# Kernel optimization log

Hardware: AMD Instinct MI355X
Metric: run time of the kernel (lower is better)

Reference implementation:

```python
import jax, jax.numpy as jnp
import numpy as np

N, E, D = 100000, 640000, 128  # nodes, edges, feature dim (in_dim == out_dim == 128)
BN_EPS = 1e-5


def setup_inputs() -> dict:
    key = jax.random.key(0)
    ks = jax.random.split(key, 8)
    x = jax.random.normal(ks[0], (N, D), dtype=jnp.float32)
    edge_index = jax.random.randint(ks[1], (2, E), 0, N, dtype=jnp.int64)
    s = 1.0 / np.sqrt(D)
    W1 = jax.random.uniform(ks[2], (D, D), jnp.float32, -s, s)
    b1 = jax.random.uniform(ks[3], (D,), jnp.float32, -s, s)
    W2 = jax.random.uniform(ks[4], (D, D), jnp.float32, -s, s)
    b2 = jax.random.uniform(ks[5], (D,), jnp.float32, -s, s)
    return {
        "x": x,
        "edge_index": edge_index,
        "eps": jnp.array([0.1], dtype=jnp.float32),
        "W1": W1, "b1": b1,
        "g1": jnp.ones((D,), jnp.float32), "beta1": jnp.zeros((D,), jnp.float32),
        "W2": W2, "b2": b2,
        "g2": jnp.ones((D,), jnp.float32), "beta2": jnp.zeros((D,), jnp.float32),
    }


def _batchnorm(h, gamma, beta):
    # BatchNorm1d in training mode: biased batch stats over the node dim
    mean = jnp.mean(h, axis=0)
    var = jnp.var(h, axis=0)
    return gamma * (h - mean) * jax.lax.rsqrt(var + BN_EPS) + beta


def reference(x, edge_index, eps, W1, b1, g1, beta1, W2, b2, g2, beta2):
    src, dst = edge_index[0], edge_index[1]
    # gather messages from source nodes, scatter-add into destination nodes
    aggr = jax.ops.segment_sum(x[src], dst, num_segments=x.shape[0])  # [N, D]
    h = (1.0 + eps) * x + aggr
    h = jax.nn.relu(_batchnorm(h @ W1.T + b1, g1, beta1))
    h = jax.nn.relu(_batchnorm(h @ W2.T + b2, g2, beta2))
    return h
```

## Files before the change

kernel.cpp:

```cpp
#include <hip/hip_runtime.h>

#define NN 100000
#define DD 128
#define EE 640000
#define NPAD 100352

typedef __bf16 bf16x8 __attribute__((ext_vector_type(8)));
typedef float floatx4 __attribute__((ext_vector_type(4)));

__device__ __forceinline__ unsigned short f2bf(float f) {
    unsigned int u = __float_as_uint(f);
    u += 0x7FFF + ((u >> 16) & 1);
    return (unsigned short)(u >> 16);
}

__global__ __launch_bounds__(256) void hist_k(const int* __restrict__ ei,
                                              int* __restrict__ deg) {
    int e = blockIdx.x * 256 + threadIdx.x;
    if (e < EE) atomicAdd(&deg[ei[EE + e]], 1);
}

__global__ __launch_bounds__(256) void scan1_k(const int* __restrict__ deg,
                                               int* __restrict__ exc,
                                               int* __restrict__ chunkSums) {
    __shared__ int s[256];
    int t = threadIdx.x, g = blockIdx.x * 256 + t;
    int v = (g < NN) ? deg[g] : 0;
    s[t] = v;
    __syncthreads();
    for (int off = 1; off < 256; off <<= 1) {
        int u = (t >= off) ? s[t - off] : 0;
        __syncthreads();
        s[t] += u;
        __syncthreads();
    }
    if (g < NN) exc[g] = s[t] - v;
    if (t == 255) chunkSums[blockIdx.x] = s[255];
}

__global__ __launch_bounds__(512) void scan2_k(int* __restrict__ chunkSums, int n) {
    __shared__ int s[512];
    int t = threadIdx.x;
    int v = (t < n) ? chunkSums[t] : 0;
    s[t] = v;
    __syncthreads();
    for (int off = 1; off < 512; off <<= 1) {
        int u = (t >= off) ? s[t - off] : 0;
        __syncthreads();
        s[t] += u;
        __syncthreads();
    }
    if (t < n) chunkSums[t] = s[t] - v;
}

__global__ __launch_bounds__(256) void scan3_k(int* __restrict__ exc,
                                               const int* __restrict__ chunkSums,
                                               int* __restrict__ cursor) {
    int g = blockIdx.x * 256 + threadIdx.x;
    if (g < NN) {
        int o = exc[g] + chunkSums[blockIdx.x];
        exc[g] = o;
        cursor[g] = o;
    }
}

__global__ __launch_bounds__(256) void esort_k(const int* __restrict__ ei,
                                               int* __restrict__ cursor,
                                               int* __restrict__ ssrc) {
    int e = blockIdx.x * 256 + threadIdx.x;
    if (e >= EE) return;
    int pos = atomicAdd(&cursor[ei[EE + e]], 1);
    ssrc[pos] = ei[e];
}

__global__ __launch_bounds__(256) void aggregate_k(
    const float4* __restrict__ x4, const int* __restrict__ ssrc,
    const int* __restrict__ offs, const int* __restrict__ deg,
    const float* __restrict__ epsp, ushort4* __restrict__ hout) {
    int tid = blockIdx.x * 256 + threadIdx.x;
    int node = tid >> 5, lane = tid & 31;
    if (node >= NN) return;
    int start = offs[node], d = deg[node];
    float ef = 1.0f + epsp[0];
    float4 v = x4[node * 32 + lane];
    float4 acc = make_float4(ef * v.x, ef * v.y, ef * v.z, ef * v.w);
    for (int j = 0; j < d; ++j) {
        int s = ssrc[start + j];
        float4 xv = x4[s * 32 + lane];
        acc.x += xv.x; acc.y += xv.y; acc.z += xv.z; acc.w += xv.w;
    }
    ushort4 u;
    u.x = f2bf(acc.x); u.y = f2bf(acc.y); u.z = f2bf(acc.z); u.w = f2bf(acc.w);
    hout[node * 32 + lane] = u;
}

__global__ __launch_bounds__(256, 2) void gin_gemm_k(
    const unsigned short* __restrict__ hin,
    const float* __restrict__ W, const float* __restrict__ bias,
    float* __restrict__ y, float* __restrict__ stats) {
    __shared__ __align__(16) unsigned short Ah[128][136];
    __shared__ __align__(16) unsigned short Bw[128][136];
    __shared__ __align__(16) float s_sum[128];
    __shared__ __align__(16) float s_sq[128];

    const int tid = threadIdx.x;
    const int rowBase = blockIdx.x * 128;

    if (tid < 128) { s_sum[tid] = 0.f; s_sq[tid] = 0.f; }

    const float4* W4 = (const float4*)W;
#pragma unroll
    for (int j = 0; j < 16; ++j) {
        int f4 = j * 256 + tid;
        int row = f4 >> 5, k4 = f4 & 31;
        float4 wv = W4[f4];
        ushort4 u;
        u.x = f2bf(wv.x); u.y = f2bf(wv.y); u.z = f2bf(wv.z); u.w = f2bf(wv.w);
        *(ushort4*)&Bw[row][k4 * 4] = u;
    }

    const int4* h16 = (const int4*)hin;
#pragma unroll
    for (int j = 0; j < 8; ++j) {
        int c = j * 256 + tid;
        int row = c >> 4, c8 = c & 15;
        int rg = rowBase + row;
        int4 v = make_int4(0, 0, 0, 0);
        if (rg < NN) v = h16[rg * 16 + c8];
        *(int4*)&Ah[row][c8 * 8] = v;
    }

    __syncthreads();

    const int l = tid & 63, w = tid >> 6;
    const int m = l & 15, q = l >> 4;

    floatx4 acc[2][8];
#pragma unroll
    for (int rt = 0; rt < 2; ++rt)
#pragma unroll
        for (int ct = 0; ct < 8; ++ct) acc[rt][ct] = (floatx4)0.0f;

#pragma unroll
    for (int kc = 0; kc < 4; ++kc) {
        int k0 = kc * 32 + q * 8;
        bf16x8 a0 = *(const bf16x8*)&Ah[w * 32 + m][k0];
        bf16x8 a1 = *(const bf16x8*)&Ah[w * 32 + 16 + m][k0];
#pragma unroll
        for (int ct = 0; ct < 8; ++ct) {
            bf16x8 b = *(const bf16x8*)&Bw[ct * 16 + m][k0];
            acc[0][ct] = __builtin_amdgcn_mfma_f32_16x16x32_bf16(a0, b, acc[0][ct], 0, 0, 0);
            acc[1][ct] = __builtin_amdgcn_mfma_f32_16x16x32_bf16(a1, b, acc[1][ct], 0, 0, 0);
        }
    }

#pragma unroll
    for (int ct = 0; ct < 8; ++ct) {
        int col = ct * 16 + m;
        float bc = bias[col];
        float ps = 0.f, pq = 0.f;
#pragma unroll
        for (int rt = 0; rt < 2; ++rt) {
#pragma unroll
            for (int i = 0; i < 4; ++i) {
                int rg = rowBase + w * 32 + rt * 16 + q * 4 + i;
                if (rg < NN) {
                    float yv = acc[rt][ct][i] + bc;
                    y[rg * 128 + col] = yv;
                    ps += yv;
                    pq += yv * yv;
                }
            }
        }
        atomicAdd(&s_sum[col], ps);
        atomicAdd(&s_sq[col], pq);
    }
    __syncthreads();
    if (tid < 128) {
        unsafeAtomicAdd(&stats[tid], s_sum[tid]);
        unsafeAtomicAdd(&stats[128 + tid], s_sq[tid]);
    }
}

template <int OUT_BF16>
__global__ __launch_bounds__(256) void bn_relu_k(
    const float* __restrict__ y, const float* __restrict__ stats,
    const float* __restrict__ g, const float* __restrict__ beta,
    float* outf, unsigned short* __restrict__ outh) {
    __shared__ __align__(16) float sc[128];
    __shared__ __align__(16) float sh[128];
    int t = threadIdx.x;
    if (t < 128) {
        const float inv = 1.0f / (float)NN;
        float mean = stats[t] * inv;
        float var = stats[128 + t] * inv - mean * mean;
        float s = g[t] * rsqrtf(var + 1e-5f);
        sc[t] = s;
        sh[t] = beta[t] - mean * s;
    }
    __syncthreads();
    const int total4 = NN * 32;
    const float4* y4 = (const float4*)y;
    for (int i = blockIdx.x * 256 + t; i < total4; i += gridDim.x * 256) {
        int c4 = i & 31;
        float4 v = y4[i];
        float4 s = ((const float4*)sc)[c4];
        float4 b = ((const float4*)sh)[c4];
        float r0 = fmaxf(v.x * s.x + b.x, 0.f);
        float r1 = fmaxf(v.y * s.y + b.y, 0.f);
        float r2 = fmaxf(v.z * s.z + b.z, 0.f);
        float r3 = fmaxf(v.w * s.w + b.w, 0.f);
        if (OUT_BF16) {
            ushort4 u;
            u.x = f2bf(r0); u.y = f2bf(r1); u.z = f2bf(r2); u.w = f2bf(r3);
            ((ushort4*)outh)[i] = u;
        } else {
            ((float4*)outf)[i] = make_float4(r0, r1, r2, r3);
        }
    }
}

extern "C" void kernel_launch(void* const* d_in, const int* in_sizes, int n_in,
                              void* d_out, int out_size, void* d_ws, size_t ws_size,
                              hipStream_t stream) {
    const float* x   = (const float*)d_in[0];
    const int* ei    = (const int*)d_in[1];
    const float* W1  = (const float*)d_in[3];
    const float* b1  = (const float*)d_in[4];
    const float* g1  = (const float*)d_in[5];
    const float* be1 = (const float*)d_in[6];
    const float* W2  = (const float*)d_in[7];
    const float* b2  = (const float*)d_in[8];
    const float* g2  = (const float*)d_in[9];
    const float* be2 = (const float*)d_in[10];
    const float* eps = (const float*)d_in[2];
    float* out = (float*)d_out;

    int* deg        = (int*)d_ws;
    int* offs       = deg + NPAD;
    int* cursor     = offs + NPAD;
    int* chunkSums  = cursor + NPAD;
    int* ssrc       = chunkSums + 512;
    unsigned short* hbuf = (unsigned short*)(ssrc + EE + 256);
    float* stats    = (float*)(hbuf + (size_t)NN * DD);

    hipMemsetAsync(deg, 0, NPAD * sizeof(int), stream);
    hipMemsetAsync(stats, 0, 512 * sizeof(float), stream);

    const int numChunks = (NN + 255) / 256;
    hist_k<<<(EE + 255) / 256, 256, 0, stream>>>(ei, deg);
    scan1_k<<<numChunks, 256, 0, stream>>>(deg, offs, chunkSums);
    scan2_k<<<1, 512, 0, stream>>>(chunkSums, numChunks);
    scan3_k<<<numChunks, 256, 0, stream>>>(offs, chunkSums, cursor);
    esort_k<<<(EE + 255) / 256, 256, 0, stream>>>(ei, cursor, ssrc);
    aggregate_k<<<(NN * 32 + 255) / 256, 256, 0, stream>>>(
        (const float4*)x, ssrc, offs, deg, eps, (ushort4*)hbuf);

    int gblocks = (NN + 127) / 128;
    gin_gemm_k<<<gblocks, 256, 0, stream>>>(hbuf, W1, b1, out, stats);
    bn_relu_k<1><<<4096, 256, 0, stream>>>(out, stats, g1, be1, nullptr, hbuf);
    gin_gemm_k<<<gblocks, 256, 0, stream>>>(hbuf, W2, b2, out, stats + 256);
    bn_relu_k<0><<<4096, 256, 0, stream>>>(out, stats + 256, g2, be2, out, nullptr);
}
```

Baseline: 361.2 us.

## Fuse first BN+ReLU into second GEMM load and unroll gather by four

```diff
diff --git a/kernel.cpp b/kernel.cpp
--- a/kernel.cpp
+++ b/kernel.cpp
@@ -83,30 +83,62 @@
     int start = offs[node], d = deg[node];
     float ef = 1.0f + epsp[0];
     float4 v = x4[node * 32 + lane];
-    float4 acc = make_float4(ef * v.x, ef * v.y, ef * v.z, ef * v.w);
-    for (int j = 0; j < d; ++j) {
-        int s = ssrc[start + j];
-        float4 xv = x4[s * 32 + lane];
-        acc.x += xv.x; acc.y += xv.y; acc.z += xv.z; acc.w += xv.w;
+    float ax = ef * v.x, ay = ef * v.y, az = ef * v.z, aw = ef * v.w;
+    for (int j = 0; j < d; j += 4) {
+        int r = d - j;
+        int b = start + j;
+        int s0 = ssrc[b];
+        int s1 = ssrc[b + ((r > 1) ? 1 : 0)];
+        int s2 = ssrc[b + ((r > 2) ? 2 : 0)];
+        int s3 = ssrc[b + ((r > 3) ? 3 : 0)];
+        float4 xa = x4[s0 * 32 + lane];
+        float4 xb = x4[s1 * 32 + lane];
+        float4 xc = x4[s2 * 32 + lane];
+        float4 xd = x4[s3 * 32 + lane];
+        float m1 = (r > 1) ? 1.f : 0.f;
+        float m2 = (r > 2) ? 1.f : 0.f;
+        float m3 = (r > 3) ? 1.f : 0.f;
+        ax += xa.x; ay += xa.y; az += xa.z; aw += xa.w;
+        ax += m1 * xb.x; ay += m1 * xb.y; az += m1 * xb.z; aw += m1 * xb.w;
+        ax += m2 * xc.x; ay += m2 * xc.y; az += m2 * xc.z; aw += m2 * xc.w;
+        ax += m3 * xd.x; ay += m3 * xd.y; az += m3 * xd.z; aw += m3 * xd.w;
     }
     ushort4 u;
-    u.x = f2bf(acc.x); u.y = f2bf(acc.y); u.z = f2bf(acc.z); u.w = f2bf(acc.w);
+    u.x = f2bf(ax); u.y = f2bf(ay); u.z = f2bf(az); u.w = f2bf(aw);
     hout[node * 32 + lane] = u;
 }
 
+template <int FUSE_BN>
 __global__ __launch_bounds__(256, 2) void gin_gemm_k(
     const unsigned short* __restrict__ hin,
+    const float* __restrict__ yin,
+    const float* __restrict__ statsIn,
+    const float* __restrict__ gmm,
+    const float* __restrict__ bta,
     const float* __restrict__ W, const float* __restrict__ bias,
-    float* __restrict__ y, float* __restrict__ stats) {
+    float* __restrict__ y, float* __restrict__ statsOut) {
     __shared__ __align__(16) unsigned short Ah[128][136];
     __shared__ __align__(16) unsigned short Bw[128][136];
     __shared__ __align__(16) float s_sum[128];
     __shared__ __align__(16) float s_sq[128];
+    __shared__ __align__(16) float sc[128];
+    __shared__ __align__(16) float sh[128];
 
     const int tid = threadIdx.x;
     const int rowBase = blockIdx.x * 128;
 
-    if (tid < 128) { s_sum[tid] = 0.f; s_sq[tid] = 0.f; }
+    if (tid < 128) {
+        s_sum[tid] = 0.f;
+        s_sq[tid] = 0.f;
+        if (FUSE_BN) {
+            const float inv = 1.0f / (float)NN;
+            float mean = statsIn[tid] * inv;
+            float var = statsIn[128 + tid] * inv - mean * mean;
+            float s = gmm[tid] * rsqrtf(var + 1e-5f);
+            sc[tid] = s;
+            sh[tid] = bta[tid] - mean * s;
+        }
+    }
 
     const float4* W4 = (const float4*)W;
 #pragma unroll
@@ -119,15 +151,37 @@
         *(ushort4*)&Bw[row][k4 * 4] = u;
     }
 
-    const int4* h16 = (const int4*)hin;
-#pragma unroll
-    for (int j = 0; j < 8; ++j) {
-        int c = j * 256 + tid;
-        int row = c >> 4, c8 = c & 15;
-        int rg = rowBase + row;
-        int4 v = make_int4(0, 0, 0, 0);
-        if (rg < NN) v = h16[rg * 16 + c8];
-        *(int4*)&Ah[row][c8 * 8] = v;
+    if (FUSE_BN) {
+        __syncthreads();
+        const float4* y4in = (const float4*)yin;
+#pragma unroll
+        for (int j = 0; j < 16; ++j) {
+            int c = j * 256 + tid;
+            int row = c >> 5, c4 = c & 31;
+            int rg = rowBase + row;
+            ushort4 u = make_ushort4(0, 0, 0, 0);
+            if (rg < NN) {
+                float4 v = y4in[rg * 32 + c4];
+                float4 s4 = ((const float4*)sc)[c4];
+                float4 b4 = ((const float4*)sh)[c4];
+                u.x = f2bf(fmaxf(v.x * s4.x + b4.x, 0.f));
+                u.y = f2bf(fmaxf(v.y * s4.y + b4.y, 0.f));
+                u.z = f2bf(fmaxf(v.z * s4.z + b4.z, 0.f));
+                u.w = f2bf(fmaxf(v.w * s4.w + b4.w, 0.f));
+            }
+            *(ushort4*)&Ah[row][c4 * 4] = u;
+        }
+    } else {
+        const int4* h16 = (const int4*)hin;
+#pragma unroll
+        for (int j = 0; j < 8; ++j) {
+            int c = j * 256 + tid;
+            int row = c >> 4, c8 = c & 15;
+            int rg = rowBase + row;
+            int4 v = make_int4(0, 0, 0, 0);
+            if (rg < NN) v = h16[rg * 16 + c8];
+            *(int4*)&Ah[row][c8 * 8] = v;
+        }
     }
 
     __syncthreads();
@@ -177,8 +231,8 @@
     }
     __syncthreads();
     if (tid < 128) {
-        unsafeAtomicAdd(&stats[tid], s_sum[tid]);
-        unsafeAtomicAdd(&stats[128 + tid], s_sq[tid]);
+        unsafeAtomicAdd(&statsOut[tid], s_sum[tid]);
+        unsafeAtomicAdd(&statsOut[128 + tid], s_sq[tid]);
     }
 }
 
@@ -225,6 +279,7 @@
                               hipStream_t stream) {
     const float* x   = (const float*)d_in[0];
     const int* ei    = (const int*)d_in[1];
+    const float* eps = (const float*)d_in[2];
     const float* W1  = (const float*)d_in[3];
     const float* b1  = (const float*)d_in[4];
     const float* g1  = (const float*)d_in[5];
@@ -233,7 +288,6 @@
     const float* b2  = (const float*)d_in[8];
     const float* g2  = (const float*)d_in[9];
     const float* be2 = (const float*)d_in[10];
-    const float* eps = (const float*)d_in[2];
     float* out = (float*)d_out;
 
     int* deg        = (int*)d_ws;
@@ -243,6 +297,9 @@
     int* ssrc       = chunkSums + 512;
     unsigned short* hbuf = (unsigned short*)(ssrc + EE + 256);
     float* stats    = (float*)(hbuf + (size_t)NN * DD);
+    float* ybuf     = stats + 512;
+    size_t need     = (size_t)((char*)(ybuf + (size_t)NN * DD) - (char*)d_ws);
+    const bool fused = ws_size >= need;
 
     hipMemsetAsync(deg, 0, NPAD * sizeof(int), stream);
     hipMemsetAsync(stats, 0, 512 * sizeof(float), stream);
@@ -257,8 +314,18 @@
         (const float4*)x, ssrc, offs, deg, eps, (ushort4*)hbuf);
 
     int gblocks = (NN + 127) / 128;
-    gin_gemm_k<<<gblocks, 256, 0, stream>>>(hbuf, W1, b1, out, stats);
-    bn_relu_k<1><<<4096, 256, 0, stream>>>(out, stats, g1, be1, nullptr, hbuf);
-    gin_gemm_k<<<gblocks, 256, 0, stream>>>(hbuf, W2, b2, out, stats + 256);
-    bn_relu_k<0><<<4096, 256, 0, stream>>>(out, stats + 256, g2, be2, out, nullptr);
-}
+    if (fused) {
+        gin_gemm_k<0><<<gblocks, 256, 0, stream>>>(
+            hbuf, nullptr, nullptr, nullptr, nullptr, W1, b1, ybuf, stats);
+        gin_gemm_k<1><<<gblocks, 256, 0, stream>>>(
+            nullptr, ybuf, stats, g1, be1, W2, b2, out, stats + 256);
+        bn_relu_k<0><<<4096, 256, 0, stream>>>(out, stats + 256, g2, be2, out, nullptr);
+    } else {
+        gin_gemm_k<0><<<gblocks, 256, 0, stream>>>(
+            hbuf, nullptr, nullptr, nullptr, nullptr, W1, b1, out, stats);
+        bn_relu_k<1><<<4096, 256, 0, stream>>>(out, stats, g1, be1, nullptr, hbuf);
+        gin_gemm_k<0><<<gblocks, 256, 0, stream>>>(
+            hbuf, nullptr, nullptr, nullptr, nullptr, W2, b2, out, stats + 256);
+        bn_relu_k<0><<<4096, 256, 0, stream>>>(out, stats + 256, g2, be2, out, nullptr);
+    }
+}
```

Result: faster. 345.1 us (-4.4%).

## Persistent register-resident-weight GEMM, prebaked bf16 weights, 4-way unrolled gather

Applied to the files above, without the earlier changes.

```diff
diff --git a/kernel.cpp b/kernel.cpp
--- a/kernel.cpp
+++ b/kernel.cpp
@@ -7,6 +7,12 @@
 
 typedef __bf16 bf16x8 __attribute__((ext_vector_type(8)));
 typedef float floatx4 __attribute__((ext_vector_type(4)));
+
+union BF8 {
+    bf16x8 v;
+    unsigned short u[8];
+    int4 i4;
+};
 
 __device__ __forceinline__ unsigned short f2bf(float f) {
     unsigned int u = __float_as_uint(f);
@@ -71,6 +77,17 @@
     if (e >= EE) return;
     int pos = atomicAdd(&cursor[ei[EE + e]], 1);
     ssrc[pos] = ei[e];
+}
+
+__global__ __launch_bounds__(256) void wconv_k(const float* __restrict__ W1,
+                                               const float* __restrict__ W2,
+                                               unsigned short* __restrict__ wb) {
+    int i = blockIdx.x * 256 + threadIdx.x;
+    const float4* s4 = (i < 4096) ? (const float4*)W1 : (const float4*)W2;
+    float4 v = s4[i & 4095];
+    ushort4 u;
+    u.x = f2bf(v.x); u.y = f2bf(v.y); u.z = f2bf(v.z); u.w = f2bf(v.w);
+    ((ushort4*)wb)[i] = u;
 }
 
 __global__ __launch_bounds__(256) void aggregate_k(
@@ -83,102 +100,122 @@
     int start = offs[node], d = deg[node];
     float ef = 1.0f + epsp[0];
     float4 v = x4[node * 32 + lane];
-    float4 acc = make_float4(ef * v.x, ef * v.y, ef * v.z, ef * v.w);
-    for (int j = 0; j < d; ++j) {
-        int s = ssrc[start + j];
-        float4 xv = x4[s * 32 + lane];
-        acc.x += xv.x; acc.y += xv.y; acc.z += xv.z; acc.w += xv.w;
+    float ax = ef * v.x, ay = ef * v.y, az = ef * v.z, aw = ef * v.w;
+    for (int j = 0; j < d; j += 4) {
+        int r = d - j;
+        int b = start + j;
+        int s0 = ssrc[b];
+        int s1 = ssrc[b + ((r > 1) ? 1 : 0)];
+        int s2 = ssrc[b + ((r > 2) ? 2 : 0)];
+        int s3 = ssrc[b + ((r > 3) ? 3 : 0)];
+        float4 xa = x4[s0 * 32 + lane];
+        float4 xb = x4[s1 * 32 + lane];
+        float4 xc = x4[s2 * 32 + lane];
+        float4 xd = x4[s3 * 32 + lane];
+        float m1 = (r > 1) ? 1.f : 0.f;
+        float m2 = (r > 2) ? 1.f : 0.f;
+        float m3 = (r > 3) ? 1.f : 0.f;
+        ax += xa.x; ay += xa.y; az += xa.z; aw += xa.w;
+        ax += m1 * xb.x; ay += m1 * xb.y; az += m1 * xb.z; aw += m1 * xb.w;
+        ax += m2 * xc.x; ay += m2 * xc.y; az += m2 * xc.z; aw += m2 * xc.w;
+        ax += m3 * xd.x; ay += m3 * xd.y; az += m3 * xd.z; aw += m3 * xd.w;
     }
     ushort4 u;
-    u.x = f2bf(acc.x); u.y = f2bf(acc.y); u.z = f2bf(acc.z); u.w = f2bf(acc.w);
+    u.x = f2bf(ax); u.y = f2bf(ay); u.z = f2bf(az); u.w = f2bf(aw);
     hout[node * 32 + lane] = u;
 }
 
 __global__ __launch_bounds__(256, 2) void gin_gemm_k(
     const unsigned short* __restrict__ hin,
-    const float* __restrict__ W, const float* __restrict__ bias,
-    float* __restrict__ y, float* __restrict__ stats) {
-    __shared__ __align__(16) unsigned short Ah[128][136];
-    __shared__ __align__(16) unsigned short Bw[128][136];
+    const unsigned short* __restrict__ Wbf, const float* __restrict__ bias,
+    float* __restrict__ y, float* __restrict__ statsOut) {
     __shared__ __align__(16) float s_sum[128];
     __shared__ __align__(16) float s_sq[128];
 
     const int tid = threadIdx.x;
-    const int rowBase = blockIdx.x * 128;
-
-    if (tid < 128) { s_sum[tid] = 0.f; s_sq[tid] = 0.f; }
-
-    const float4* W4 = (const float4*)W;
-#pragma unroll
-    for (int j = 0; j < 16; ++j) {
-        int f4 = j * 256 + tid;
-        int row = f4 >> 5, k4 = f4 & 31;
-        float4 wv = W4[f4];
-        ushort4 u;
-        u.x = f2bf(wv.x); u.y = f2bf(wv.y); u.z = f2bf(wv.z); u.w = f2bf(wv.w);
-        *(ushort4*)&Bw[row][k4 * 4] = u;
-    }
-
-    const int4* h16 = (const int4*)hin;
-#pragma unroll
-    for (int j = 0; j < 8; ++j) {
-        int c = j * 256 + tid;
-        int row = c >> 4, c8 = c & 15;
-        int rg = rowBase + row;
-        int4 v = make_int4(0, 0, 0, 0);
-        if (rg < NN) v = h16[rg * 16 + c8];
-        *(int4*)&Ah[row][c8 * 8] = v;
-    }
-
-    __syncthreads();
-
     const int l = tid & 63, w = tid >> 6;
     const int m = l & 15, q = l >> 4;
 
-    floatx4 acc[2][8];
-#pragma unroll
-    for (int rt = 0; rt < 2; ++rt)
-#pragma unroll
-        for (int ct = 0; ct < 8; ++ct) acc[rt][ct] = (floatx4)0.0f;
-
-#pragma unroll
-    for (int kc = 0; kc < 4; ++kc) {
-        int k0 = kc * 32 + q * 8;
-        bf16x8 a0 = *(const bf16x8*)&Ah[w * 32 + m][k0];
-        bf16x8 a1 = *(const bf16x8*)&Ah[w * 32 + 16 + m][k0];
+    if (tid < 128) { s_sum[tid] = 0.f; s_sq[tid] = 0.f; }
+
+    bf16x8 wf[8][4];
+#pragma unroll
+    for (int ct = 0; ct < 8; ++ct) {
+        const unsigned short* wr = Wbf + (size_t)(ct * 16 + m) * 128 + q * 8;
+#pragma unroll
+        for (int kc = 0; kc < 4; ++kc) {
+            BF8 t;
+            t.i4 = *(const int4*)(wr + kc * 32);
+            wf[ct][kc] = t.v;
+        }
+    }
+    float bc[8];
+#pragma unroll
+    for (int ct = 0; ct < 8; ++ct) bc[ct] = bias[ct * 16 + m];
+
+    float ps[8], pq[8];
+#pragma unroll
+    for (int ct = 0; ct < 8; ++ct) { ps[ct] = 0.f; pq[ct] = 0.f; }
+
+    __syncthreads();
+
+    const int NT = NN / 16;
+    const int stride = gridDim.x * 4;
+    int t = blockIdx.x * 4 + w;
+
+    const unsigned short* abase = hin + (size_t)m * 128 + q * 8;
+
+    int4 ra[4];
+    if (t < NT) {
+        const unsigned short* ap = abase + (size_t)t * (16 * 128);
+#pragma unroll
+        for (int kc = 0; kc < 4; ++kc) ra[kc] = *(const int4*)(ap + kc * 32);
+    }
+
+    while (t < NT) {
+        bf16x8 a[4];
+#pragma unroll
+        for (int kc = 0; kc < 4; ++kc) { BF8 tt; tt.i4 = ra[kc]; a[kc] = tt.v; }
+
+        int tn = t + stride;
+        if (tn < NT) {
+            const unsigned short* ap = abase + (size_t)tn * (16 * 128);
+#pragma unroll
+            for (int kc = 0; kc < 4; ++kc) ra[kc] = *(const int4*)(ap + kc * 32);
+        }
+
+        floatx4 acc[8];
+#pragma unroll
+        for (int ct = 0; ct < 8; ++ct) acc[ct] = (floatx4)0.0f;
+#pragma unroll
+        for (int kc = 0; kc < 4; ++kc)
+#pragma unroll
+            for (int ct = 0; ct < 8; ++ct)
+                acc[ct] = __builtin_amdgcn_mfma_f32_16x16x32_bf16(a[kc], wf[ct][kc], acc[ct], 0, 0, 0);
+
+        float* yb = y + (size_t)(t * 16 + q * 4) * 128 + m;
 #pragma unroll
         for (int ct = 0; ct < 8; ++ct) {
-            bf16x8 b = *(const bf16x8*)&Bw[ct * 16 + m][k0];
-            acc[0][ct] = __builtin_amdgcn_mfma_f32_16x16x32_bf16(a0, b, acc[0][ct], 0, 0, 0);
-            acc[1][ct] = __builtin_amdgcn_mfma_f32_16x16x32_bf16(a1, b, acc[1][ct], 0, 0, 0);
-        }
-    }
-
-#pragma unroll
-    for (int ct = 0; ct < 8; ++ct) {
-        int col = ct * 16 + m;
-        float bc = bias[col];
-        float ps = 0.f, pq = 0.f;
-#pragma unroll
-        for (int rt = 0; rt < 2; ++rt) {
 #pragma unroll
             for (int i = 0; i < 4; ++i) {
-                int rg = rowBase + w * 32 + rt * 16 + q * 4 + i;
-                if (rg < NN) {
-                    float yv = acc[rt][ct][i] + bc;
-                    y[rg * 128 + col] = yv;
-                    ps += yv;
-                    pq += yv * yv;
-                }
+                float yv = acc[ct][i] + bc[ct];
+                yb[(size_t)i * 128 + ct * 16] = yv;
+                ps[ct] += yv;
+                pq[ct] += yv * yv;
             }
         }
-        atomicAdd(&s_sum[col], ps);
-        atomicAdd(&s_sq[col], pq);
+        t = tn;
+    }
+
+#pragma unroll
+    for (int ct = 0; ct < 8; ++ct) {
+        atomicAdd(&s_sum[ct * 16 + m], ps[ct]);
+        atomicAdd(&s_sq[ct * 16 + m], pq[ct]);
     }
     __syncthreads();
     if (tid < 128) {
-        unsafeAtomicAdd(&stats[tid], s_sum[tid]);
-        unsafeAtomicAdd(&stats[128 + tid], s_sq[tid]);
+        unsafeAtomicAdd(&statsOut[tid], s_sum[tid]);
+        unsafeAtomicAdd(&statsOut[128 + tid], s_sq[tid]);
     }
 }
 
@@ -225,6 +262,7 @@
                               hipStream_t stream) {
     const float* x   = (const float*)d_in[0];
     const int* ei    = (const int*)d_in[1];
+    const float* eps = (const float*)d_in[2];
     const float* W1  = (const float*)d_in[3];
     const float* b1  = (const float*)d_in[4];
     const float* g1  = (const float*)d_in[5];
@@ -233,7 +271,6 @@
     const float* b2  = (const float*)d_in[8];
     const float* g2  = (const float*)d_in[9];
     const float* be2 = (const float*)d_in[10];
-    const float* eps = (const float*)d_in[2];
     float* out = (float*)d_out;
 
     int* deg        = (int*)d_ws;
@@ -243,6 +280,7 @@
     int* ssrc       = chunkSums + 512;
     unsigned short* hbuf = (unsigned short*)(ssrc + EE + 256);
     float* stats    = (float*)(hbuf + (size_t)NN * DD);
+    unsigned short* wbf = (unsigned short*)(stats + 512);
 
     hipMemsetAsync(deg, 0, NPAD * sizeof(int), stream);
     hipMemsetAsync(stats, 0, 512 * sizeof(float), stream);
@@ -255,10 +293,11 @@
     esort_k<<<(EE + 255) / 256, 256, 0, stream>>>(ei, cursor, ssrc);
     aggregate_k<<<(NN * 32 + 255) / 256, 256, 0, stream>>>(
         (const float4*)x, ssrc, offs, deg, eps, (ushort4*)hbuf);
-
-    int gblocks = (NN + 127) / 128;
-    gin_gemm_k<<<gblocks, 256, 0, stream>>>(hbuf, W1, b1, out, stats);
+    wconv_k<<<32, 256, 0, stream>>>(W1, W2, wbf);
+
+    const int gblocks = 512;
+    gin_gemm_k<<<gblocks, 256, 0, stream>>>(hbuf, wbf, b1, out, stats);
     bn_relu_k<1><<<4096, 256, 0, stream>>>(out, stats, g1, be1, nullptr, hbuf);
-    gin_gemm_k<<<gblocks, 256, 0, stream>>>(hbuf, W2, b2, out, stats + 256);
+    gin_gemm_k<<<gblocks, 256, 0, stream>>>(hbuf, wbf + 16384, b2, out, stats + 256);
     bn_relu_k<0><<<4096, 256, 0, stream>>>(out, stats + 256, g2, be2, out, nullptr);
 }
```

New measurement: 321.0 us. 1.13x faster.
